# Kernel optimization log

Measured on AMD Instinct MI355X. Metric: run time of the kernel, lower is better.

The kernel has to match this reference:

```python
import jax, jax.numpy as jnp
import numpy as np

N_EMBD = 1024
N_HEADS = 16
HEAD_SIZE = N_EMBD // N_HEADS
B, T = 2, 2048


def setup_inputs() -> dict:
    key = jax.random.key(0)
    ks = jax.random.split(key, 6)
    s_in = 1.0 / np.sqrt(N_EMBD)
    x = jax.random.normal(ks[0], (B, T, N_EMBD), dtype=jnp.float32)
    # per-head projection weights, stored (H, C, Dh) = x @ W per head
    wq = jax.random.uniform(ks[1], (N_HEADS, N_EMBD, HEAD_SIZE), dtype=jnp.float32, minval=-s_in, maxval=s_in)
    wk = jax.random.uniform(ks[2], (N_HEADS, N_EMBD, HEAD_SIZE), dtype=jnp.float32, minval=-s_in, maxval=s_in)
    wv = jax.random.uniform(ks[3], (N_HEADS, N_EMBD, HEAD_SIZE), dtype=jnp.float32, minval=-s_in, maxval=s_in)
    # output projection (in, out) layout plus bias
    w_proj = jax.random.uniform(ks[4], (N_EMBD, N_EMBD), dtype=jnp.float32, minval=-s_in, maxval=s_in)
    b_proj = jax.random.uniform(ks[5], (N_EMBD,), dtype=jnp.float32, minval=-s_in, maxval=s_in)
    return {"x": x, "wq": wq, "wk": wk, "wv": wv, "w_proj": w_proj, "b_proj": b_proj}


def reference(x, wq, wk, wv, w_proj, b_proj):
    Bb, Tt, C = x.shape
    # all-head QKV projections in one einsum each: (B,T,C)x(H,C,Dh)->(B,H,T,Dh)
    q = jnp.einsum('btc,hcd->bhtd', x, wq)
    k = jnp.einsum('btc,hcd->bhtd', x, wk)
    v = jnp.einsum('btc,hcd->bhtd', x, wv)
    # NOTE: original scales by C**-0.5 with C = full n_embd, not head_size
    scores = jnp.einsum('bhtd,bhsd->bhts', q, k) * (C ** -0.5)
    causal = jnp.tril(jnp.ones((Tt, Tt), dtype=bool))  # is_decoder=True
    scores = jnp.where(causal, scores, -jnp.inf)
    wei = jax.nn.softmax(scores, axis=-1)
    out = jnp.einsum('bhts,bhsd->bhtd', wei, v)
    # concat heads: (B,H,T,Dh) -> (B,T,H*Dh)
    out = out.transpose(0, 2, 1, 3).reshape(Bb, Tt, C)
    return out @ w_proj + b_proj
```

## Files before the change

kernel.cpp:

```cpp
#include <hip/hip_runtime.h>


typedef unsigned short u16;
typedef unsigned int u32;

using bf16x8 = __attribute__((ext_vector_type(8))) short;
using bf16x4 = __attribute__((ext_vector_type(4))) short;
using f32x4  = __attribute__((ext_vector_type(4))) float;

#define T_SEQ 2048
#define C_DIM 1024
#define H_NUM 16
#define D_HEAD 64
#define NCHUNK 30

static __device__ inline f32x4 mfma16(bf16x8 a, bf16x8 b, f32x4 c) {
  return __builtin_amdgcn_mfma_f32_16x16x32_bf16(a, b, c, 0, 0, 0);
}

static __device__ inline short f2bf(float f) {
  union { float f; u32 u; } v; v.f = f;
  u32 u = v.u;
  return (short)((u + 0x7FFFu + ((u >> 16) & 1u)) >> 16);
}

static __device__ inline float bf2f(short s) {
  union { u32 u; float f; } v; v.u = ((u32)(u16)s) << 16;
  return v.f;
}

static __device__ inline void gload_lds16(const short* g, short* l) {
  __builtin_amdgcn_global_load_lds(
      (const __attribute__((address_space(1))) unsigned int*)g,
      (__attribute__((address_space(3))) unsigned int*)l,
      16, 0, 0);
}

__global__ __launch_bounds__(256) void ingest_kernel(
    const float* __restrict__ x, const float* __restrict__ wq,
    const float* __restrict__ wk, const float* __restrict__ wv,
    const float* __restrict__ wproj,
    short* __restrict__ xb, short* __restrict__ wt, short* __restrict__ wpT) {
  const int bid = blockIdx.x, t = threadIdx.x;
  if (bid < 4096) {
    size_t i4 = ((size_t)bid * 256 + t) * 4;
    const float4 v = *(const float4*)(x + i4);
    bf16x4 o4;
    o4[0] = f2bf(v.x); o4[1] = f2bf(v.y); o4[2] = f2bf(v.z); o4[3] = f2bf(v.w);
    *(bf16x4*)(xb + i4) = o4;
    return;
  }
  __shared__ short lt[64][72];
  const int rl = t >> 2, q16 = (t & 3) * 16;
  if (bid < 4864) {
    const int wb = bid - 4096;
    const int h3 = wb >> 4, c0 = (wb & 15) * 64;
    const float* w = (h3 < 16) ? wq : (h3 < 32) ? wk : wv;
    const int h = h3 & 15;
    const float* rp = w + (size_t)h * 65536 + (size_t)(c0 + rl) * 64 + q16;
#pragma unroll
    for (int j = 0; j < 16; j++) lt[rl][q16 + j] = f2bf(rp[j]);
    __syncthreads();
    short* op = wt + (size_t)h3 * 65536 + (size_t)rl * 1024 + c0 + q16;
#pragma unroll
    for (int j = 0; j < 16; j++) op[j] = lt[q16 + j][rl];
  } else {
    const int wc = bid - 4864;
    const int k0 = (wc >> 4) * 64, n0 = (wc & 15) * 64;
    const float* rp = wproj + (size_t)(k0 + rl) * 1024 + n0 + q16;
#pragma unroll
    for (int j = 0; j < 16; j++) lt[rl][q16 + j] = f2bf(rp[j]);
    __syncthreads();
    short* op = wpT + (size_t)(n0 + rl) * 1024 + k0 + q16;
#pragma unroll
    for (int j = 0; j < 16; j++) op[j] = lt[q16 + j][rl];
  }
}

__global__ __launch_bounds__(256) void qkv_kernel(
    const short* __restrict__ x, const short* __restrict__ wt,
    short* __restrict__ qo, short* __restrict__ ko, short* __restrict__ vto) {
  const int m0 = blockIdx.x * 128;
  const int n0 = blockIdx.y * 128;
  const int tid = threadIdx.x, w = tid >> 6, lane = tid & 63;
  const int l15 = lane & 15, quad = lane >> 4;
  const int wm = w >> 1, wn = w & 1;

  __shared__ __align__(16) short As[2][128 * 32];
  __shared__ __align__(16) short Bs[2][128 * 32];

  const int srow = w * 32 + (lane >> 2);
  const int skof = (lane & 3) * 8;
  const short* ga0 = x  + (size_t)(m0 + srow) * 1024 + skof;
  const short* ga1 = ga0 + 16 * 1024;
  const short* gb0 = wt + (size_t)(n0 + srow) * 1024 + skof;
  const short* gb1 = gb0 + 16 * 1024;
  const int lof0 = (w * 32) * 32;
  const int lof1 = (w * 32 + 16) * 32;

  f32x4 acc[4][4];
#pragma unroll
  for (int i = 0; i < 4; i++)
#pragma unroll
    for (int j = 0; j < 4; j++) acc[i][j] = f32x4{0, 0, 0, 0};

  const bool isv = (n0 >= 2048);

  auto stage = [&](int bi, int kt) {
    const int k0 = kt * 32;
    gload_lds16(ga0 + k0, &As[bi][lof0]);
    gload_lds16(ga1 + k0, &As[bi][lof1]);
    gload_lds16(gb0 + k0, &Bs[bi][lof0]);
    gload_lds16(gb1 + k0, &Bs[bi][lof1]);
  };
  auto compute = [&](int bi) {
    const short* ard = &As[bi][(wm * 64 + l15) * 32 + quad * 8];
    const short* brd = &Bs[bi][(wn * 64 + l15) * 32 + quad * 8];
    bf16x8 af[4], bfr[4];
#pragma unroll
    for (int i = 0; i < 4; i++) {
      af[i]  = *(const bf16x8*)(ard + i * 16 * 32);
      bfr[i] = *(const bf16x8*)(brd + i * 16 * 32);
    }
    if (!isv) {
#pragma unroll
      for (int mi = 0; mi < 4; mi++)
#pragma unroll
        for (int ni = 0; ni < 4; ni++)
          acc[mi][ni] = mfma16(af[mi], bfr[ni], acc[mi][ni]);
    } else {
#pragma unroll
      for (int ni = 0; ni < 4; ni++)
#pragma unroll
        for (int mi = 0; mi < 4; mi++)
          acc[ni][mi] = mfma16(bfr[ni], af[mi], acc[ni][mi]);
    }
  };

  stage(0, 0);
  __syncthreads();
#pragma unroll 1
  for (int kt2 = 0; kt2 < 16; kt2++) {
    stage(1, 2 * kt2 + 1);
    compute(0);
    __syncthreads();
    if (kt2 < 15) stage(0, 2 * kt2 + 2);
    compute(1);
    __syncthreads();
  }

  const int chunk = (n0 >> 6) + wn;
  const int sel = chunk >> 4, h = chunk & 15;
  if (!isv) {
    short* outp = (sel == 0) ? qo : ko;
    const float sc = (sel == 0) ? 0.03125f : 1.0f;
#pragma unroll
    for (int mi = 0; mi < 4; mi++) {
#pragma unroll
      for (int r = 0; r < 4; r++) {
        int tg = m0 + wm * 64 + mi * 16 + quad * 4 + r;
        int b = tg >> 11, tl = tg & 2047;
        size_t rowb = ((size_t)(b * H_NUM + h) * T_SEQ + tl) * D_HEAD;
#pragma unroll
        for (int ni = 0; ni < 4; ni++)
          outp[rowb + ni * 16 + l15] = f2bf(acc[mi][ni][r] * sc);
      }
    }
  } else {
#pragma unroll
    for (int ni = 0; ni < 4; ni++) {
#pragma unroll
      for (int r = 0; r < 4; r++) {
        int d = ni * 16 + quad * 4 + r;
#pragma unroll
        for (int mi = 0; mi < 4; mi++) {
          int tg = m0 + wm * 64 + mi * 16 + l15;
          int b = tg >> 11, tl = tg & 2047;
          vto[((size_t)(b * H_NUM + h) * D_HEAD + d) * T_SEQ + tl] =
              f2bf(acc[ni][mi][r]);
        }
      }
    }
  }
}

__global__ __launch_bounds__(256) void attn_part_kernel(
    const short* __restrict__ q, const short* __restrict__ k,
    const short* __restrict__ vt, short* __restrict__ po,
    float* __restrict__ pl) {
  static const unsigned char order[NCHUNK] = {
      5, 6, 8, 10, 12, 14, 16, 17, 18, 19, 21, 22, 24, 25, 27, 28,
      4, 15,
      3, 13, 29,
      2, 11, 26,
      1, 9, 23,
      0, 7, 20};
  static const unsigned char qtb_of[NCHUNK] = {
      0, 1, 2, 3, 4, 5, 6, 6, 7, 7, 8, 8, 9, 9, 10, 10, 11, 11,
      12, 12, 12, 13, 13, 13, 14, 14, 14, 15, 15, 15};
  static const unsigned char base30[16] = {0, 1, 2, 3, 4, 5, 6, 8,
                                           10, 12, 14, 16, 18, 21, 24, 27};
  const int id = blockIdx.x;
  const int hb = id & 31;
  const int p  = id >> 5;
  const int pblk = order[p];
  const int qtb = qtb_of[pblk];
  const int sbeg = (pblk - base30[qtb]) * 768;
  const int send = min(sbeg + 768, (qtb + 1) * 128);

  const size_t bh = (size_t)hb;
  const short* qp = q  + bh * T_SEQ * D_HEAD;
  const short* kp = k  + bh * T_SEQ * D_HEAD;
  const short* vp = vt + bh * D_HEAD * T_SEQ;

  const int tid = threadIdx.x;
  const int wid = tid >> 6;
  const int lane = tid & 63;
  const int l15 = lane & 15, quad = lane >> 4;

  __shared__ __align__(16) short P_lds[4][32][72];
  short (*pq)[72] = P_lds[wid];

  const int q0w = qtb * 128 + wid * 32;
  const int s_hi = min(send, ((q0w + 95) >> 6) << 6);

  bf16x8 qa[2][2];
#pragma unroll
  for (int h2 = 0; h2 < 2; h2++)
#pragma unroll
    for (int c2 = 0; c2 < 2; c2++)
      qa[h2][c2] = *(const bf16x8*)(qp + (size_t)(q0w + h2 * 16 + l15) * D_HEAD
                                    + c2 * 32 + quad * 8);

  f32x4 o[2][4];
#pragma unroll
  for (int h2 = 0; h2 < 2; h2++)
#pragma unroll
    for (int c = 0; c < 4; c++) o[h2][c] = f32x4{0, 0, 0, 0};
  float l_i[2] = { 0.f, 0.f };

  bf16x8 ka[4][2];
#pragma unroll
  for (int c = 0; c < 4; c++) {
    const short* krow = kp + (size_t)(sbeg + c * 16 + l15) * D_HEAD + quad * 8;
    ka[c][0] = *(const bf16x8*)(krow);
    ka[c][1] = *(const bf16x8*)(krow + 32);
  }

#pragma unroll 1
  for (int s0 = sbeg; s0 < s_hi; s0 += 64) {
    bf16x8 va[2][4];
#pragma unroll
    for (int kb2 = 0; kb2 < 2; kb2++)
#pragma unroll
      for (int c = 0; c < 4; c++)
        va[kb2][c] = *(const bf16x8*)(vp + (size_t)(c * 16 + l15) * T_SEQ
                                      + s0 + kb2 * 32 + quad * 8);

    f32x4 s[2][4];
#pragma unroll
    for (int c = 0; c < 4; c++) {
#pragma unroll
      for (int h2 = 0; h2 < 2; h2++) {
        f32x4 z = { 0, 0, 0, 0 };
        z = mfma16(ka[c][0], qa[h2][0], z);
        z = mfma16(ka[c][1], qa[h2][1], z);
        s[h2][c] = z;
      }
    }

    const int s0n = (s0 + 64 < s_hi) ? (s0 + 64) : s0;
#pragma unroll
    for (int c = 0; c < 4; c++) {
      const short* krow = kp + (size_t)(s0n + c * 16 + l15) * D_HEAD + quad * 8;
      ka[c][0] = *(const bf16x8*)(krow);
      ka[c][1] = *(const bf16x8*)(krow + 32);
    }

    const bool needMask = (s0 + 64 > q0w);
#pragma unroll
    for (int h2 = 0; h2 < 2; h2++) {
      const int qg = q0w + h2 * 16 + l15;
      if (needMask) {
#pragma unroll
        for (int c = 0; c < 4; c++)
#pragma unroll
          for (int r = 0; r < 4; r++)
            if (s0 + c * 16 + quad * 4 + r > qg) s[h2][c][r] = -1e30f;
      }
      float rs = 0.f;
#pragma unroll
      for (int c = 0; c < 4; c++) {
#pragma unroll
        for (int r = 0; r < 4; r++) {
          float p2 = __expf(s[h2][c][r]);
          s[h2][c][r] = p2;
          rs += p2;
        }
      }
      l_i[h2] += rs;
#pragma unroll
      for (int c = 0; c < 4; c++) {
        bf16x4 pk;
        pk[0] = f2bf(s[h2][c][0]); pk[1] = f2bf(s[h2][c][1]);
        pk[2] = f2bf(s[h2][c][2]); pk[3] = f2bf(s[h2][c][3]);
        *(bf16x4*)(&pq[h2 * 16 + l15][c * 16 + quad * 4]) = pk;
      }
    }
    asm volatile("" ::: "memory");

#pragma unroll
    for (int kb2 = 0; kb2 < 2; kb2++) {
      bf16x8 pb[2];
      pb[0] = *(const bf16x8*)(&pq[l15][kb2 * 32 + quad * 8]);
      pb[1] = *(const bf16x8*)(&pq[16 + l15][kb2 * 32 + quad * 8]);
#pragma unroll
      for (int c = 0; c < 4; c++) {
        o[0][c] = mfma16(va[kb2][c], pb[0], o[0][c]);
        o[1][c] = mfma16(va[kb2][c], pb[1], o[1][c]);
      }
    }
    asm volatile("" ::: "memory");
  }

  const size_t prow = (bh * NCHUNK + pblk) * 128;
#pragma unroll
  for (int h2 = 0; h2 < 2; h2++) {
    float lsum = l_i[h2];
    lsum += __shfl_xor(lsum, 16);
    lsum += __shfl_xor(lsum, 32);
    float inv = 1.0f / lsum;
    int qlocal = wid * 32 + h2 * 16 + l15;
    size_t rowoff = (prow + qlocal) * 64;
#pragma unroll
    for (int c = 0; c < 4; c++) {
      bf16x4 ok;
      ok[0] = f2bf(o[h2][c][0] * inv); ok[1] = f2bf(o[h2][c][1] * inv);
      ok[2] = f2bf(o[h2][c][2] * inv); ok[3] = f2bf(o[h2][c][3] * inv);
      *(bf16x4*)(&po[rowoff + c * 16 + quad * 4]) = ok;
    }
    if (quad == 0) pl[prow + qlocal] = lsum;
  }
}

__global__ __launch_bounds__(256) void attn_merge_kernel(
    const short* __restrict__ po, const float* __restrict__ pl,
    short* __restrict__ attnb) {
  static const unsigned char base30[16] = {0, 1, 2, 3, 4, 5, 6, 8,
                                           10, 12, 14, 16, 18, 21, 24, 27};
  int id = blockIdx.x * 256 + threadIdx.x;
  int dg = id & 7;
  int h  = (id >> 3) & 15;
  int t  = (id >> 7) & 2047;
  int b  = id >> 18;
  int qtb = t >> 7, ql = t & 127;
  int nch = 1 + (qtb >= 6) + (qtb >= 12);
  size_t bh = (size_t)(b * H_NUM + h);
  size_t r0 = (bh * NCHUNK + base30[qtb]) * 128 + ql;
  bf16x8 res;
  if (nch == 1) {
    res = *(const bf16x8*)(po + r0 * 64 + dg * 8);
  } else {
    float acc[8] = {0, 0, 0, 0, 0, 0, 0, 0};
    float lsum = 0.f;
    for (int c = 0; c < nch; c++) {
      size_t r = r0 + (size_t)c * 128;
      float lc = pl[r];
      lsum += lc;
      bf16x8 p = *(const bf16x8*)(po + r * 64 + dg * 8);
#pragma unroll
      for (int j = 0; j < 8; j++) acc[j] += lc * bf2f(p[j]);
    }
    float inv = 1.0f / lsum;
#pragma unroll
    for (int j = 0; j < 8; j++) res[j] = f2bf(acc[j] * inv);
  }
  *(bf16x8*)(&attnb[((size_t)(b * T_SEQ + t)) * C_DIM + h * D_HEAD + dg * 8]) = res;
}

__global__ __launch_bounds__(256) void proj_kernel(
    const short* __restrict__ a_in, const short* __restrict__ wpT,
    const float* __restrict__ bias, float* __restrict__ out) {
  const int m0 = blockIdx.x * 128;
  const int n0 = blockIdx.y * 128;
  const int tid = threadIdx.x, w = tid >> 6, lane = tid & 63;
  const int l15 = lane & 15, quad = lane >> 4;
  const int wm = w >> 1, wn = w & 1;

  __shared__ __align__(16) short As[2][128 * 32];
  __shared__ __align__(16) short Bs[2][128 * 32];

  const int srow = w * 32 + (lane >> 2);
  const int skof = (lane & 3) * 8;
  const short* ga0 = a_in + (size_t)(m0 + srow) * 1024 + skof;
  const short* ga1 = ga0 + 16 * 1024;
  const short* gb0 = wpT + (size_t)(n0 + srow) * 1024 + skof;
  const short* gb1 = gb0 + 16 * 1024;
  const int lof0 = (w * 32) * 32;
  const int lof1 = (w * 32 + 16) * 32;

  f32x4 acc[4][4];
#pragma unroll
  for (int i = 0; i < 4; i++)
#pragma unroll
    for (int j = 0; j < 4; j++) acc[i][j] = f32x4{0, 0, 0, 0};

  auto stage = [&](int bi, int kt) {
    const int k0 = kt * 32;
    gload_lds16(ga0 + k0, &As[bi][lof0]);
    gload_lds16(ga1 + k0, &As[bi][lof1]);
    gload_lds16(gb0 + k0, &Bs[bi][lof0]);
    gload_lds16(gb1 + k0, &Bs[bi][lof1]);
  };
  auto compute = [&](int bi) {
    const short* ard = &As[bi][(wm * 64 + l15) * 32 + quad * 8];
    const short* brd = &Bs[bi][(wn * 64 + l15) * 32 + quad * 8];
    bf16x8 af[4], bfr[4];
#pragma unroll
    for (int i = 0; i < 4; i++) {
      af[i]  = *(const bf16x8*)(ard + i * 16 * 32);
      bfr[i] = *(const bf16x8*)(brd + i * 16 * 32);
    }
#pragma unroll
    for (int mi = 0; mi < 4; mi++)
#pragma unroll
      for (int ni = 0; ni < 4; ni++)
        acc[mi][ni] = mfma16(af[mi], bfr[ni], acc[mi][ni]);
  };

  stage(0, 0);
  __syncthreads();
#pragma unroll 1
  for (int kt2 = 0; kt2 < 16; kt2++) {
    stage(1, 2 * kt2 + 1);
    compute(0);
    __syncthreads();
    if (kt2 < 15) stage(0, 2 * kt2 + 2);
    compute(1);
    __syncthreads();
  }

#pragma unroll
  for (int mi = 0; mi < 4; mi++) {
#pragma unroll
    for (int r = 0; r < 4; r++) {
      int mq = m0 + wm * 64 + mi * 16 + quad * 4 + r;
#pragma unroll
      for (int ni = 0; ni < 4; ni++) {
        int n = n0 + wn * 64 + ni * 16 + l15;
        out[(size_t)mq * C_DIM + n] = acc[mi][ni][r] + bias[n];
      }
    }
  }
}

extern "C" void kernel_launch(void* const* d_in, const int* in_sizes, int n_in,
                              void* d_out, int out_size, void* d_ws, size_t ws_size,
                              hipStream_t stream) {
  const float* x     = (const float*)d_in[0];
  const float* wq    = (const float*)d_in[1];
  const float* wk    = (const float*)d_in[2];
  const float* wv    = (const float*)d_in[3];
  const float* wproj = (const float*)d_in[4];
  const float* bias  = (const float*)d_in[5];

  short* ws = (short*)d_ws;
  short* wpT    = ws;
  short* qb     = ws + 1048576;
  short* wt_qkv = ws + 9437184;
  short* xb     = ws + 12582912;
  short* po     = ws + 5242880;
  float* pl     = (float*)(ws + 15728640);
  short* attnb  = ws + 1048576;
  short* kb     = (short*)d_out;
  short* vtb    = (short*)d_out + 4194304;

  ingest_kernel<<<5120, 256, 0, stream>>>(x, wq, wk, wv, wproj, xb, wt_qkv, wpT);
  qkv_kernel<<<dim3(32, 24), 256, 0, stream>>>(xb, wt_qkv, qb, kb, vtb);
  attn_part_kernel<<<NCHUNK * 32, 256, 0, stream>>>(qb, kb, vtb, po, pl);
  attn_merge_kernel<<<2048, 256, 0, stream>>>(po, pl, attnb);
  proj_kernel<<<dim3(32, 8), 256, 0, stream>>>(attnb, wpT, bias, (float*)d_out);
}
```

Baseline: 234.7 us.

## Rebalance causal attention work into 41 segments packed into 128-thread blocks

The split-KV attention decomposition changes from 30 fixed chunks per head to 41 variable-length key segments. The segments are packed into 32 per-pair chunk lists, and each 2-wave block walks one list sequentially. The blocks are halved to 128 threads and the grid grows to 2048, with the aim of evening out per-block work across the causal triangle and filling more CUs. The merge kernel gets new segment base and count tables, and the partial-sum buffer offset moves. The cost is more partial outputs to write and merge, plus a serial segment loop per block.

```diff
diff --git a/kernel.cpp b/kernel.cpp
--- a/kernel.cpp
+++ b/kernel.cpp
@@ -12,7 +12,7 @@
 #define C_DIM 1024
 #define H_NUM 16
 #define D_HEAD 64
-#define NCHUNK 30
+#define NSEG 41
 
 static __device__ inline f32x4 mfma16(bf16x8 a, bf16x8 b, f32x4 c) {
   return __builtin_amdgcn_mfma_f32_16x16x32_bf16(a, b, c, 0, 0, 0);
@@ -184,29 +184,29 @@
   }
 }
 
-__global__ __launch_bounds__(256) void attn_part_kernel(
+__global__ __launch_bounds__(128) void attn_part_kernel(
     const short* __restrict__ q, const short* __restrict__ k,
     const short* __restrict__ vt, short* __restrict__ po,
     float* __restrict__ pl) {
-  static const unsigned char order[NCHUNK] = {
-      5, 6, 8, 10, 12, 14, 16, 17, 18, 19, 21, 22, 24, 25, 27, 28,
-      4, 15,
-      3, 13, 29,
-      2, 11, 26,
-      1, 9, 23,
-      0, 7, 20};
-  static const unsigned char qtb_of[NCHUNK] = {
-      0, 1, 2, 3, 4, 5, 6, 6, 7, 7, 8, 8, 9, 9, 10, 10, 11, 11,
-      12, 12, 12, 13, 13, 13, 14, 14, 14, 15, 15, 15};
-  static const unsigned char base30[16] = {0, 1, 2, 3, 4, 5, 6, 8,
-                                           10, 12, 14, 16, 18, 21, 24, 27};
+  static const unsigned char cst[33] = {
+      0, 3, 5, 7, 9, 11, 12, 14, 15, 16, 17, 18, 19, 21, 22, 23, 24,
+      25, 26, 27, 28, 29, 30, 31, 32, 34, 35, 36, 37, 38, 39, 40, 41};
+  static const unsigned char seg_qtb[NSEG] = {
+      0, 1, 2, 2, 3, 3, 4, 4, 5, 5, 6, 6, 6, 7, 7, 8, 8, 9, 9, 9,
+      10, 10, 10, 11, 11, 11, 12, 12, 12, 13, 13, 13, 13, 14, 14, 14, 14,
+      15, 15, 15, 15};
+  static const unsigned short seg_s0[NSEG] = {
+      0, 0, 0, 192, 0, 384, 0, 448, 0, 384, 0, 192, 768, 0, 448, 0, 576,
+      0, 576, 1152, 0, 384, 896, 0, 512, 1024, 0, 576, 1152, 0, 576, 1152,
+      1664, 0, 384, 896, 1408, 0, 512, 1024, 1536};
+  static const unsigned char seg_nt[NSEG] = {
+      2, 4, 3, 3, 6, 2, 7, 3, 6, 6, 3, 9, 2, 7, 9, 9, 9, 9, 9, 2,
+      6, 8, 8, 8, 8, 8, 9, 9, 8, 9, 9, 8, 2, 6, 8, 8, 8, 8, 8, 8, 8};
+
   const int id = blockIdx.x;
   const int hb = id & 31;
   const int p  = id >> 5;
-  const int pblk = order[p];
-  const int qtb = qtb_of[pblk];
-  const int sbeg = (pblk - base30[qtb]) * 768;
-  const int send = min(sbeg + 768, (qtb + 1) * 128);
+  const int pair = p & 1, chunk = p >> 1;
 
   const size_t bh = (size_t)hb;
   const short* qp = q  + bh * T_SEQ * D_HEAD;
@@ -217,146 +217,156 @@
   const int wid = tid >> 6;
   const int lane = tid & 63;
   const int l15 = lane & 15, quad = lane >> 4;
-
-  __shared__ __align__(16) short P_lds[4][32][72];
+  const int w4 = pair * 2 + wid;
+
+  __shared__ __align__(16) short P_lds[2][32][72];
   short (*pq)[72] = P_lds[wid];
 
-  const int q0w = qtb * 128 + wid * 32;
-  const int s_hi = min(send, ((q0w + 95) >> 6) << 6);
-
-  bf16x8 qa[2][2];
-#pragma unroll
-  for (int h2 = 0; h2 < 2; h2++)
-#pragma unroll
-    for (int c2 = 0; c2 < 2; c2++)
-      qa[h2][c2] = *(const bf16x8*)(qp + (size_t)(q0w + h2 * 16 + l15) * D_HEAD
-                                    + c2 * 32 + quad * 8);
-
-  f32x4 o[2][4];
-#pragma unroll
-  for (int h2 = 0; h2 < 2; h2++)
-#pragma unroll
-    for (int c = 0; c < 4; c++) o[h2][c] = f32x4{0, 0, 0, 0};
-  float l_i[2] = { 0.f, 0.f };
-
-  bf16x8 ka[4][2];
-#pragma unroll
-  for (int c = 0; c < 4; c++) {
-    const short* krow = kp + (size_t)(sbeg + c * 16 + l15) * D_HEAD + quad * 8;
-    ka[c][0] = *(const bf16x8*)(krow);
-    ka[c][1] = *(const bf16x8*)(krow + 32);
-  }
-
+  const int sfirst = cst[chunk], slast = cst[chunk + 1];
 #pragma unroll 1
-  for (int s0 = sbeg; s0 < s_hi; s0 += 64) {
-    bf16x8 va[2][4];
-#pragma unroll
-    for (int kb2 = 0; kb2 < 2; kb2++)
-#pragma unroll
-      for (int c = 0; c < 4; c++)
-        va[kb2][c] = *(const bf16x8*)(vp + (size_t)(c * 16 + l15) * T_SEQ
-                                      + s0 + kb2 * 32 + quad * 8);
-
-    f32x4 s[2][4];
+  for (int si = sfirst; si < slast; ++si) {
+    const int qtb = seg_qtb[si];
+    const int sbeg = seg_s0[si];
+    const int send = sbeg + seg_nt[si] * 64;
+    const int q0w = qtb * 128 + w4 * 32;
+    const int s_hi = min(send, ((q0w + 95) >> 6) << 6);
+
+    bf16x8 qa[2][2];
+#pragma unroll
+    for (int h2 = 0; h2 < 2; h2++)
+#pragma unroll
+      for (int c2 = 0; c2 < 2; c2++)
+        qa[h2][c2] = *(const bf16x8*)(qp + (size_t)(q0w + h2 * 16 + l15) * D_HEAD
+                                      + c2 * 32 + quad * 8);
+
+    f32x4 o[2][4];
+#pragma unroll
+    for (int h2 = 0; h2 < 2; h2++)
+#pragma unroll
+      for (int c = 0; c < 4; c++) o[h2][c] = f32x4{0, 0, 0, 0};
+    float l_i[2] = { 0.f, 0.f };
+
+    bf16x8 ka[4][2];
 #pragma unroll
     for (int c = 0; c < 4; c++) {
-#pragma unroll
-      for (int h2 = 0; h2 < 2; h2++) {
-        f32x4 z = { 0, 0, 0, 0 };
-        z = mfma16(ka[c][0], qa[h2][0], z);
-        z = mfma16(ka[c][1], qa[h2][1], z);
-        s[h2][c] = z;
-      }
-    }
-
-    const int s0n = (s0 + 64 < s_hi) ? (s0 + 64) : s0;
-#pragma unroll
-    for (int c = 0; c < 4; c++) {
-      const short* krow = kp + (size_t)(s0n + c * 16 + l15) * D_HEAD + quad * 8;
+      const short* krow = kp + (size_t)(sbeg + c * 16 + l15) * D_HEAD + quad * 8;
       ka[c][0] = *(const bf16x8*)(krow);
       ka[c][1] = *(const bf16x8*)(krow + 32);
     }
 
-    const bool needMask = (s0 + 64 > q0w);
+#pragma unroll 1
+    for (int s0 = sbeg; s0 < s_hi; s0 += 64) {
+      bf16x8 va[2][4];
+#pragma unroll
+      for (int kb2 = 0; kb2 < 2; kb2++)
+#pragma unroll
+        for (int c = 0; c < 4; c++)
+          va[kb2][c] = *(const bf16x8*)(vp + (size_t)(c * 16 + l15) * T_SEQ
+                                        + s0 + kb2 * 32 + quad * 8);
+
+      f32x4 s[2][4];
+#pragma unroll
+      for (int c = 0; c < 4; c++) {
+#pragma unroll
+        for (int h2 = 0; h2 < 2; h2++) {
+          f32x4 z = { 0, 0, 0, 0 };
+          z = mfma16(ka[c][0], qa[h2][0], z);
+          z = mfma16(ka[c][1], qa[h2][1], z);
+          s[h2][c] = z;
+        }
+      }
+
+      const int s0n = (s0 + 64 < s_hi) ? (s0 + 64) : s0;
+#pragma unroll
+      for (int c = 0; c < 4; c++) {
+        const short* krow = kp + (size_t)(s0n + c * 16 + l15) * D_HEAD + quad * 8;
+        ka[c][0] = *(const bf16x8*)(krow);
+        ka[c][1] = *(const bf16x8*)(krow + 32);
+      }
+
+      const bool needMask = (s0 + 64 > q0w);
+#pragma unroll
+      for (int h2 = 0; h2 < 2; h2++) {
+        const int qg = q0w + h2 * 16 + l15;
+        if (needMask) {
+#pragma unroll
+          for (int c = 0; c < 4; c++)
+#pragma unroll
+            for (int r = 0; r < 4; r++)
+              if (s0 + c * 16 + quad * 4 + r > qg) s[h2][c][r] = -1e30f;
+        }
+        float rs = 0.f;
+#pragma unroll
+        for (int c = 0; c < 4; c++) {
+#pragma unroll
+          for (int r = 0; r < 4; r++) {
+            float p2 = __expf(s[h2][c][r]);
+            s[h2][c][r] = p2;
+            rs += p2;
+          }
+        }
+        l_i[h2] += rs;
+#pragma unroll
+        for (int c = 0; c < 4; c++) {
+          bf16x4 pk;
+          pk[0] = f2bf(s[h2][c][0]); pk[1] = f2bf(s[h2][c][1]);
+          pk[2] = f2bf(s[h2][c][2]); pk[3] = f2bf(s[h2][c][3]);
+          *(bf16x4*)(&pq[h2 * 16 + l15][c * 16 + quad * 4]) = pk;
+        }
+      }
+      asm volatile("" ::: "memory");
+
+#pragma unroll
+      for (int kb2 = 0; kb2 < 2; kb2++) {
+        bf16x8 pb[2];
+        pb[0] = *(const bf16x8*)(&pq[l15][kb2 * 32 + quad * 8]);
+        pb[1] = *(const bf16x8*)(&pq[16 + l15][kb2 * 32 + quad * 8]);
+#pragma unroll
+        for (int c = 0; c < 4; c++) {
+          o[0][c] = mfma16(va[kb2][c], pb[0], o[0][c]);
+          o[1][c] = mfma16(va[kb2][c], pb[1], o[1][c]);
+        }
+      }
+      asm volatile("" ::: "memory");
+    }
+
+    const size_t prow = (bh * NSEG + si) * 128;
 #pragma unroll
     for (int h2 = 0; h2 < 2; h2++) {
-      const int qg = q0w + h2 * 16 + l15;
-      if (needMask) {
-#pragma unroll
-        for (int c = 0; c < 4; c++)
-#pragma unroll
-          for (int r = 0; r < 4; r++)
-            if (s0 + c * 16 + quad * 4 + r > qg) s[h2][c][r] = -1e30f;
-      }
-      float rs = 0.f;
+      float lsum = l_i[h2];
+      lsum += __shfl_xor(lsum, 16);
+      lsum += __shfl_xor(lsum, 32);
+      float inv = (lsum > 0.f) ? 1.0f / lsum : 0.f;
+      int qlocal = w4 * 32 + h2 * 16 + l15;
+      size_t rowoff = (prow + qlocal) * 64;
 #pragma unroll
       for (int c = 0; c < 4; c++) {
-#pragma unroll
-        for (int r = 0; r < 4; r++) {
-          float p2 = __expf(s[h2][c][r]);
-          s[h2][c][r] = p2;
-          rs += p2;
-        }
-      }
-      l_i[h2] += rs;
-#pragma unroll
-      for (int c = 0; c < 4; c++) {
-        bf16x4 pk;
-        pk[0] = f2bf(s[h2][c][0]); pk[1] = f2bf(s[h2][c][1]);
-        pk[2] = f2bf(s[h2][c][2]); pk[3] = f2bf(s[h2][c][3]);
-        *(bf16x4*)(&pq[h2 * 16 + l15][c * 16 + quad * 4]) = pk;
-      }
-    }
-    asm volatile("" ::: "memory");
-
-#pragma unroll
-    for (int kb2 = 0; kb2 < 2; kb2++) {
-      bf16x8 pb[2];
-      pb[0] = *(const bf16x8*)(&pq[l15][kb2 * 32 + quad * 8]);
-      pb[1] = *(const bf16x8*)(&pq[16 + l15][kb2 * 32 + quad * 8]);
-#pragma unroll
-      for (int c = 0; c < 4; c++) {
-        o[0][c] = mfma16(va[kb2][c], pb[0], o[0][c]);
-        o[1][c] = mfma16(va[kb2][c], pb[1], o[1][c]);
-      }
-    }
-    asm volatile("" ::: "memory");
-  }
-
-  const size_t prow = (bh * NCHUNK + pblk) * 128;
-#pragma unroll
-  for (int h2 = 0; h2 < 2; h2++) {
-    float lsum = l_i[h2];
-    lsum += __shfl_xor(lsum, 16);
-    lsum += __shfl_xor(lsum, 32);
-    float inv = 1.0f / lsum;
-    int qlocal = wid * 32 + h2 * 16 + l15;
-    size_t rowoff = (prow + qlocal) * 64;
-#pragma unroll
-    for (int c = 0; c < 4; c++) {
-      bf16x4 ok;
-      ok[0] = f2bf(o[h2][c][0] * inv); ok[1] = f2bf(o[h2][c][1] * inv);
-      ok[2] = f2bf(o[h2][c][2] * inv); ok[3] = f2bf(o[h2][c][3] * inv);
-      *(bf16x4*)(&po[rowoff + c * 16 + quad * 4]) = ok;
-    }
-    if (quad == 0) pl[prow + qlocal] = lsum;
+        bf16x4 ok;
+        ok[0] = f2bf(o[h2][c][0] * inv); ok[1] = f2bf(o[h2][c][1] * inv);
+        ok[2] = f2bf(o[h2][c][2] * inv); ok[3] = f2bf(o[h2][c][3] * inv);
+        *(bf16x4*)(&po[rowoff + c * 16 + quad * 4]) = ok;
+      }
+      if (quad == 0) pl[prow + qlocal] = lsum;
+    }
   }
 }
 
 __global__ __launch_bounds__(256) void attn_merge_kernel(
     const short* __restrict__ po, const float* __restrict__ pl,
     short* __restrict__ attnb) {
-  static const unsigned char base30[16] = {0, 1, 2, 3, 4, 5, 6, 8,
-                                           10, 12, 14, 16, 18, 21, 24, 27};
+  static const unsigned char mseg0[16] = {0, 1, 2, 4, 6, 8, 10, 13,
+                                          15, 17, 20, 23, 26, 29, 33, 37};
+  static const unsigned char mcnt[16]  = {1, 1, 2, 2, 2, 2, 3, 2,
+                                          2, 3, 3, 3, 3, 4, 4, 4};
   int id = blockIdx.x * 256 + threadIdx.x;
   int dg = id & 7;
   int h  = (id >> 3) & 15;
   int t  = (id >> 7) & 2047;
   int b  = id >> 18;
   int qtb = t >> 7, ql = t & 127;
-  int nch = 1 + (qtb >= 6) + (qtb >= 12);
+  int nch = mcnt[qtb];
   size_t bh = (size_t)(b * H_NUM + h);
-  size_t r0 = (bh * NCHUNK + base30[qtb]) * 128 + ql;
+  size_t r0 = (bh * NSEG + mseg0[qtb]) * 128 + ql;
   bf16x8 res;
   if (nch == 1) {
     res = *(const bf16x8*)(po + r0 * 64 + dg * 8);
@@ -470,14 +480,14 @@
   short* wt_qkv = ws + 9437184;
   short* xb     = ws + 12582912;
   short* po     = ws + 5242880;
-  float* pl     = (float*)(ws + 15728640);
+  float* pl     = (float*)(ws + 15990784);
   short* attnb  = ws + 1048576;
   short* kb     = (short*)d_out;
   short* vtb    = (short*)d_out + 4194304;
 
   ingest_kernel<<<5120, 256, 0, stream>>>(x, wq, wk, wv, wproj, xb, wt_qkv, wpT);
   qkv_kernel<<<dim3(32, 24), 256, 0, stream>>>(xb, wt_qkv, qb, kb, vtb);
-  attn_part_kernel<<<NCHUNK * 32, 256, 0, stream>>>(qb, kb, vtb, po, pl);
+  attn_part_kernel<<<2048, 128, 0, stream>>>(qb, kb, vtb, po, pl);
   attn_merge_kernel<<<2048, 256, 0, stream>>>(po, pl, attnb);
   proj_kernel<<<dim3(32, 8), 256, 0, stream>>>(attnb, wpT, bias, (float*)d_out);
 }
```

Result: no change. 234.5 us (-0.1%).
